# Kernel optimization log

Hardware: AMD Instinct MI355X
Metric: run time of the kernel (lower is better)

## Reference

```python
import jax, jax.numpy as jnp
import numpy as np

N_USERS = 100000
N_MOVIES = 20000
N_EDGES = 600000
FEAT = 64
HID = 128
OUT = 64
N_TUPLES = 100000


def _sage(x_src, x_dst, src_idx, dst_idx, n_dst, Wl, bl, Wr):
    # PyG SAGEConv (mean aggr): lin_l(mean of gathered src feats) + lin_r(x_dst)
    msg = x_src[src_idx]                                        # [E, d_src]
    summ = jax.ops.segment_sum(msg, dst_idx, num_segments=n_dst)
    cnt = jax.ops.segment_sum(jnp.ones((src_idx.shape[0],), x_src.dtype),
                              dst_idx, num_segments=n_dst)
    mean = summ / jnp.maximum(cnt, 1.0)[:, None]
    return mean @ Wl.T + bl + x_dst @ Wr.T


def setup_inputs() -> dict:
    key = jax.random.key(0)
    ks = jax.random.split(key, 20)
    s = 0.05
    return {
        "movie_x": jax.random.normal(ks[0], (N_MOVIES, FEAT), jnp.float32),
        "user_idx": jax.random.randint(ks[1], (N_EDGES,), 0, N_USERS),
        "movie_idx": jax.random.randint(ks[2], (N_EDGES,), 0, N_MOVIES),
        "tuples_coo": jax.random.randint(ks[3], (2, N_TUPLES), 0, N_MOVIES),
        "user_emb": jax.random.normal(ks[4], (1, HID), jnp.float32) * s,
        "W1l": jax.random.normal(ks[5], (HID, FEAT), jnp.float32) * s,
        "b1": jnp.zeros((HID,), jnp.float32),
        "W1r": jax.random.normal(ks[6], (HID, HID), jnp.float32) * s,
        "W2l": jax.random.normal(ks[7], (HID, HID), jnp.float32) * s,
        "b2": jnp.zeros((HID,), jnp.float32),
        "W2r": jax.random.normal(ks[8], (HID, FEAT), jnp.float32) * s,
        "W3l": jax.random.normal(ks[9], (HID, HID), jnp.float32) * s,
        "b3": jnp.zeros((HID,), jnp.float32),
        "W3r": jax.random.normal(ks[10], (HID, HID), jnp.float32) * s,
        "Wlin1": jax.random.normal(ks[11], (OUT, HID), jnp.float32) * s,
        "blin1": jnp.zeros((OUT,), jnp.float32),
        "Wlin2": jax.random.normal(ks[12], (OUT, HID), jnp.float32) * s,
        "blin2": jnp.zeros((OUT,), jnp.float32),
    }


def reference(movie_x, user_idx, movie_idx, tuples_coo, user_emb,
              W1l, b1, W1r, W2l, b2, W2r, W3l, b3, W3r,
              Wlin1, blin1, Wlin2, blin2):
    n_users = N_USERS
    user_x0 = jnp.broadcast_to(user_emb, (n_users, HID))  # emb.weight.repeat
    # conv1: (movie -> user) rev_rates edges: src=movie_idx, dst=user_idx
    user_x = jax.nn.relu(_sage(movie_x, user_x0, movie_idx, user_idx, n_users, W1l, b1, W1r))
    # conv2: (user -> movie) rates edges: src=user_idx, dst=movie_idx
    movie_z = jax.nn.relu(_sage(user_x, movie_x, user_idx, movie_idx, N_MOVIES, W2l, b2, W2r))
    # conv3: (movie -> user) again
    user_z = jax.nn.relu(_sage(movie_z, user_x, movie_idx, user_idx, n_users, W3l, b3, W3r))
    z_user = user_z @ Wlin1.T + blin1
    z_movie = movie_z @ Wlin2.T + blin2
    X = jnp.vstack((z_user, z_movie))
    # relation_schema = ['user', 'movie']: offset movie indices by n_users
    new_index = jnp.vstack((tuples_coo[0], tuples_coo[1] + n_users))
    return X, new_index
```

## Files before the change

kernel.cpp:

```cpp
#include <hip/hip_runtime.h>

typedef __attribute__((ext_vector_type(8))) short short8;
typedef __attribute__((ext_vector_type(4))) float f32x4;

static const int NU = 100000;
static const int NM = 20000;
static const int NE = 600000;
static const int FEAT = 64;
static const int HID = 128;
static const int OUTD = 64;
static const int NTOT = NU + NM;
static const int CVT_TOT = 81920 + NM * FEAT;
static const int CVT_BLKS = (CVT_TOT + 255) / 256;
static const int IDX_BLKS = (100000 + 255) / 256;

static const int UB_SHIFT = 9;
static const int MB_SHIFT = 7;
static const int NBU = (NU + 511) >> 9;
static const int NBM = (NM + 127) >> 7;
static const int NBUCK = NBU + NBM;
static const int EPB = 4096;
static const int NPBLK = (NE + EPB - 1) / EPB;
static const int CAP = 8192;

__device__ inline float b2f(unsigned short h) {
    unsigned int u = ((unsigned int)h) << 16;
    float f; __builtin_memcpy(&f, &u, 4); return f;
}
__device__ inline unsigned short f2b(float f) {
    unsigned int u; __builtin_memcpy(&u, &f, 4);
    u += 0x7FFFu + ((u >> 16) & 1u);
    return (unsigned short)(u >> 16);
}
__device__ inline unsigned int pk2(float a, float b) {
    return (unsigned int)f2b(a) | ((unsigned int)f2b(b) << 16);
}
__device__ inline int wswz(int row, int bc, int rowbytes) {
    return row * rowbytes + (bc ^ ((row & 7) << 4));
}

__global__ __launch_bounds__(256) void k_part_misc(
        const int* __restrict__ ui, const int* __restrict__ mi,
        int* __restrict__ gcur, int* __restrict__ entries,
        const float* __restrict__ w1l, const float* __restrict__ w2l,
        const float* __restrict__ w2r, const float* __restrict__ w3l,
        const float* __restrict__ w3r, const float* __restrict__ wl1,
        const float* __restrict__ wl2, const float* __restrict__ mx,
        unsigned short* __restrict__ dst,
        const int* __restrict__ tpl, float* __restrict__ oidx,
        const float* __restrict__ ue, const float* __restrict__ w1r,
        const float* __restrict__ b1, float* __restrict__ c1) {
    __shared__ int h[NBUCK], base[NBUCK], cur[NBUCK];
    const int b = blockIdx.x;
    const int tid = threadIdx.x;
    if (b < NPBLK) {
        for (int i = tid; i < NBUCK; i += 256) h[i] = 0;
        __syncthreads();
        int eu[EPB / 256], em[EPB / 256];
#pragma unroll
        for (int it = 0; it < EPB / 256; ++it) {
            int e = b * EPB + it * 256 + tid;
            if (e < NE) {
                eu[it] = ui[e]; em[it] = mi[e];
                atomicAdd(&h[eu[it] >> UB_SHIFT], 1);
                atomicAdd(&h[NBU + (em[it] >> MB_SHIFT)], 1);
            } else eu[it] = -1;
        }
        __syncthreads();
        for (int i = tid; i < NBUCK; i += 256) {
            int c = h[i];
            base[i] = c ? (i * CAP + atomicAdd(&gcur[i], c)) : 0;
            cur[i] = 0;
        }
        __syncthreads();
#pragma unroll
        for (int it = 0; it < EPB / 256; ++it) {
            if (eu[it] < 0) continue;
            int u = eu[it], m = em[it];
            int bu = u >> UB_SHIFT;
            int o1 = base[bu] + atomicAdd(&cur[bu], 1);
            entries[o1] = (m << UB_SHIFT) | (u & 511);
            int bm = NBU + (m >> MB_SHIFT);
            int o2 = base[bm] + atomicAdd(&cur[bm], 1);
            entries[o2] = (u << MB_SHIFT) | (m & 127);
        }
    } else if (b < NPBLK + CVT_BLKS) {
        int g = (b - NPBLK) * 256 + tid;
        if (g >= CVT_TOT) return;
        const float* s; int o;
        if      (g < 8192)   { s = w1l; o = g; }
        else if (g < 24576)  { s = w2l; o = g - 8192; }
        else if (g < 32768)  { s = w2r; o = g - 24576; }
        else if (g < 49152)  { s = w3l; o = g - 32768; }
        else if (g < 65536)  { s = w3r; o = g - 49152; }
        else if (g < 73728)  { s = wl1; o = g - 65536; }
        else if (g < 81920)  { s = wl2; o = g - 73728; }
        else                 { s = mx;  o = g - 81920; }
        dst[g] = f2b(s[o]);
    } else if (b < NPBLK + CVT_BLKS + IDX_BLKS) {
        int i = (b - NPBLK - CVT_BLKS) * 256 + tid;
        if (i < 100000) {
            oidx[i] = (float)tpl[i];
            oidx[100000 + i] = (float)(tpl[100000 + i] + NU);
        }
    } else {
        int hh = tid;
        if (hh < HID) {
            float a = 0.f;
#pragma unroll 16
            for (int k = 0; k < HID; ++k) a += ue[k] * w1r[hh * HID + k];
            c1[hh] = a + b1[hh];
        }
    }
}

__global__ __launch_bounds__(256) void k_csr(const int* __restrict__ gcur,
                                             const int* __restrict__ entries,
                                             int2* __restrict__ rp2,
                                             int* __restrict__ list) {
    __shared__ int lcnt[512], lrp[512], lcur[512], ps[256];
    const int b = blockIdx.x;
    const int tid = threadIdx.x;
    const int s = b * CAP;
    const int e = s + gcur[b];
    const bool isU = b < NBU;
    const int shift = isU ? UB_SHIFT : MB_SHIFT;
    const int mask = isU ? 511 : 127;
    const int n0 = isU ? (b << UB_SHIFT) : ((b - NBU) << MB_SHIFT);
    const int nNodes = isU ? min(512, NU - n0) : min(128, NM - n0);
    const int g0 = isU ? n0 : NU + n0;

    for (int i = tid; i < 512; i += 256) { lcnt[i] = 0; lcur[i] = 0; }
    __syncthreads();
    for (int i = s + tid; i < e; i += 256)
        atomicAdd(&lcnt[entries[i] & mask], 1);
    __syncthreads();
    int a0 = lcnt[2 * tid], a1 = lcnt[2 * tid + 1];
    int pr = a0 + a1;
    ps[tid] = pr;
    __syncthreads();
#pragma unroll
    for (int off = 1; off < 256; off <<= 1) {
        int x = (tid >= off) ? ps[tid - off] : 0;
        __syncthreads();
        ps[tid] += x;
        __syncthreads();
    }
    int excl = ps[tid] - pr;
    lrp[2 * tid] = excl;
    lrp[2 * tid + 1] = excl + a0;
    __syncthreads();
    for (int i = tid; i < nNodes; i += 256)
        rp2[g0 + i] = make_int2(s + lrp[i], s + lrp[i] + lcnt[i]);
    for (int i = s + tid; i < e; i += 256) {
        int p = entries[i];
        int dl = p & mask;
        int off = s + lrp[dl] + atomicAdd(&lcur[dl], 1);
        list[off] = p >> shift;
    }
}

template<int C>
__global__ __launch_bounds__(256) void k_gather_b(const unsigned short* __restrict__ src,
                                                  const int2* __restrict__ rp2,
                                                  const int* __restrict__ list,
                                                  unsigned short* __restrict__ dst,
                                                  int base, int n) {
    constexpr int TPN = C / 8;
    constexpr int NPB = 256 / TPN;
    const int node = blockIdx.x * NPB + threadIdx.x / TPN;
    if (node >= n) return;
    const int c8 = (threadIdx.x % TPN) * 8;
    const int2 se = rp2[base + node];
    const int s = se.x, e = se.y;

    float a[8];
#pragma unroll
    for (int j = 0; j < 8; ++j) a[j] = 0.f;

    int i = s;
    for (; i + 3 < e; i += 4) {
        int r0 = list[i], r1 = list[i + 1], r2 = list[i + 2], r3 = list[i + 3];
        short8 v0 = *reinterpret_cast<const short8*>(src + (size_t)r0 * C + c8);
        short8 v1 = *reinterpret_cast<const short8*>(src + (size_t)r1 * C + c8);
        short8 v2 = *reinterpret_cast<const short8*>(src + (size_t)r2 * C + c8);
        short8 v3 = *reinterpret_cast<const short8*>(src + (size_t)r3 * C + c8);
#pragma unroll
        for (int j = 0; j < 8; ++j)
            a[j] += (b2f((unsigned short)v0[j]) + b2f((unsigned short)v1[j]))
                  + (b2f((unsigned short)v2[j]) + b2f((unsigned short)v3[j]));
    }
    for (; i < e; ++i) {
        int r0 = list[i];
        short8 v0 = *reinterpret_cast<const short8*>(src + (size_t)r0 * C + c8);
#pragma unroll
        for (int j = 0; j < 8; ++j) a[j] += b2f((unsigned short)v0[j]);
    }
    const float sc = 1.0f / (float)max(e - s, 1);
    short8 o;
#pragma unroll
    for (int j = 0; j < 8; ++j) o[j] = (short)f2b(a[j] * sc);
    *reinterpret_cast<short8*>(dst + (size_t)node * C + c8) = o;
}

__global__ __launch_bounds__(256) void k_gather_relu(const unsigned short* __restrict__ Y1,
                                                     const int2* __restrict__ rp2,
                                                     const int* __restrict__ list,
                                                     const float* __restrict__ c1,
                                                     unsigned short* __restrict__ user_x,
                                                     int n) {
    const int node = blockIdx.x * 16 + threadIdx.x / 16;
    if (node >= n) return;
    const int c8 = (threadIdx.x % 16) * 8;
    const int2 se = rp2[node];
    const int s = se.x, e = se.y;

    float a[8];
#pragma unroll
    for (int j = 0; j < 8; ++j) a[j] = 0.f;

    int i = s;
    for (; i + 3 < e; i += 4) {
        int r0 = list[i], r1 = list[i + 1], r2 = list[i + 2], r3 = list[i + 3];
        short8 v0 = *reinterpret_cast<const short8*>(Y1 + (size_t)r0 * HID + c8);
        short8 v1 = *reinterpret_cast<const short8*>(Y1 + (size_t)r1 * HID + c8);
        short8 v2 = *reinterpret_cast<const short8*>(Y1 + (size_t)r2 * HID + c8);
        short8 v3 = *reinterpret_cast<const short8*>(Y1 + (size_t)r3 * HID + c8);
#pragma unroll
        for (int j = 0; j < 8; ++j)
            a[j] += (b2f((unsigned short)v0[j]) + b2f((unsigned short)v1[j]))
                  + (b2f((unsigned short)v2[j]) + b2f((unsigned short)v3[j]));
    }
    for (; i < e; ++i) {
        int r0 = list[i];
        short8 v0 = *reinterpret_cast<const short8*>(Y1 + (size_t)r0 * HID + c8);
#pragma unroll
        for (int j = 0; j < 8; ++j) a[j] += b2f((unsigned short)v0[j]);
    }
    const float sc = 1.0f / (float)max(e - s, 1);
    float4 cv0 = *reinterpret_cast<const float4*>(c1 + c8);
    float4 cv1 = *reinterpret_cast<const float4*>(c1 + c8 + 4);
    float r[8];
    r[0] = fmaxf(a[0] * sc + cv0.x, 0.f); r[1] = fmaxf(a[1] * sc + cv0.y, 0.f);
    r[2] = fmaxf(a[2] * sc + cv0.z, 0.f); r[3] = fmaxf(a[3] * sc + cv0.w, 0.f);
    r[4] = fmaxf(a[4] * sc + cv1.x, 0.f); r[5] = fmaxf(a[5] * sc + cv1.y, 0.f);
    r[6] = fmaxf(a[6] * sc + cv1.z, 0.f); r[7] = fmaxf(a[7] * sc + cv1.w, 0.f);
    uint4 o;
    o.x = pk2(r[0], r[1]); o.y = pk2(r[2], r[3]);
    o.z = pk2(r[4], r[5]); o.w = pk2(r[6], r[7]);
    *reinterpret_cast<uint4*>(user_x + (size_t)node * HID + c8) = o;
}

template<int K, int NO, bool AVEC, bool RELU, bool F32OUT>
__global__ __launch_bounds__(256) void k_mf2(const unsigned short* __restrict__ X,
                                             const unsigned short* __restrict__ W,
                                             const float* __restrict__ vec,
                                             void* __restrict__ Yv, int M) {
    constexpr int KT = K / 32;
    constexpr int CG = NO / 16;
    constexpr int WB = NO * K * 2;
    constexpr int RB = K * 2;
    __shared__ __align__(16) char lds[WB];
    const int tid = threadIdx.x;
    const int lane = tid & 63;
    const int wv = tid >> 6;
    const int rbase = blockIdx.x * 128 + wv * 32;
    const int lr = lane & 15;
    const int kg = lane >> 4;

#pragma unroll
    for (int i = 0; i < WB / 16 / 256; ++i) {
        int idx = tid + i * 256;
        int row = idx / (RB / 16);
        int bc = (idx % (RB / 16)) * 16;
        *reinterpret_cast<uint4*>(lds + wswz(row, bc, RB)) =
            *reinterpret_cast<const uint4*>((const char*)W + idx * 16);
    }

    short8 xb[2][KT];
#pragma unroll
    for (int t = 0; t < 2; ++t) {
        int row = min(rbase + t * 16 + lr, M - 1);
#pragma unroll
        for (int kt = 0; kt < KT; ++kt)
            xb[t][kt] = *reinterpret_cast<const short8*>(
                X + (size_t)row * K + kt * 32 + kg * 8);
    }
    __syncthreads();

    f32x4 acc[2][CG];
#pragma unroll
    for (int t = 0; t < 2; ++t)
#pragma unroll
        for (int c = 0; c < CG; ++c) acc[t][c] = (f32x4){0.f, 0.f, 0.f, 0.f};

#pragma unroll
    for (int cg = 0; cg < CG; ++cg) {
        short8 wf[KT];
#pragma unroll
        for (int kt = 0; kt < KT; ++kt)
            wf[kt] = *reinterpret_cast<const short8*>(
                lds + wswz(cg * 16 + lr, kt * 64 + kg * 16, RB));
#pragma unroll
        for (int kt = 0; kt < KT; ++kt)
#pragma unroll
            for (int t = 0; t < 2; ++t)
                acc[t][cg] = __builtin_amdgcn_mfma_f32_16x16x32_bf16(
                    wf[kt], xb[t][kt], acc[t][cg], 0, 0, 0);
    }

#pragma unroll
    for (int t = 0; t < 2; ++t) {
        const int u = rbase + t * 16 + lr;
        if (u >= M) continue;
#pragma unroll
        for (int cg = 0; cg < CG; ++cg) {
            const int h0 = cg * 16 + kg * 4;
            float v[4];
#pragma unroll
            for (int r = 0; r < 4; ++r) v[r] = acc[t][cg][r];
            if (AVEC) {
                float4 vv = *reinterpret_cast<const float4*>(vec + h0);
                v[0] += vv.x; v[1] += vv.y; v[2] += vv.z; v[3] += vv.w;
            }
            if (RELU)
#pragma unroll
                for (int r = 0; r < 4; ++r) v[r] = fmaxf(v[r], 0.f);
            if (F32OUT) {
                float4 o = make_float4(v[0], v[1], v[2], v[3]);
                *reinterpret_cast<float4*>((float*)Yv + (size_t)u * NO + h0) = o;
            } else {
                uint2 o = make_uint2(pk2(v[0], v[1]), pk2(v[2], v[3]));
                *reinterpret_cast<uint2*>((unsigned short*)Yv + (size_t)u * NO + h0) = o;
            }
        }
    }
}

__global__ __launch_bounds__(256) void k_fused_u(
        const unsigned short* __restrict__ S3, const unsigned short* __restrict__ user_x,
        const unsigned short* __restrict__ W3r, const float* __restrict__ b3,
        const unsigned short* __restrict__ Wl1, const float* __restrict__ bl1,
        float* __restrict__ out, int M) {
    __shared__ __align__(16) char lds[49152];
    const int tid = threadIdx.x;
    const int lane = tid & 63;
    const int wv = tid >> 6;
    const int rbase = blockIdx.x * 128 + wv * 32;
    const int lr = lane & 15;
    const int kg = lane >> 4;

#pragma unroll
    for (int i = 0; i < 8; ++i) {
        int idx = tid + i * 256;
        int row = idx >> 4, bc = (idx & 15) << 4;
        *reinterpret_cast<uint4*>(lds + wswz(row, bc, 256)) =
            *reinterpret_cast<const uint4*>((const char*)W3r + idx * 16);
    }
#pragma unroll
    for (int i = 0; i < 4; ++i) {
        int idx = tid + i * 256;
        int row = idx >> 4, bc = (idx & 15) << 4;
        *reinterpret_cast<uint4*>(lds + 32768 + wswz(row, bc, 256)) =
            *reinterpret_cast<const uint4*>((const char*)Wl1 + idx * 16);
    }

    short8 xc[2][4];
#pragma unroll
    for (int t = 0; t < 2; ++t) {
        int row = min(rbase + t * 16 + lr, M - 1);
#pragma unroll
        for (int kt = 0; kt < 4; ++kt)
            xc[t][kt] = *reinterpret_cast<const short8*>(
                user_x + (size_t)row * HID + kt * 32 + kg * 8);
    }
    __syncthreads();

    f32x4 acc[2][8];
#pragma unroll
    for (int t = 0; t < 2; ++t)
#pragma unroll
        for (int c = 0; c < 8; ++c) acc[t][c] = (f32x4){0.f, 0.f, 0.f, 0.f};

#pragma unroll
    for (int cg = 0; cg < 8; ++cg) {
        short8 wr[4];
#pragma unroll
        for (int kt = 0; kt < 4; ++kt)
            wr[kt] = *reinterpret_cast<const short8*>(
                lds + wswz(cg * 16 + lr, kt * 64 + kg * 16, 256));
#pragma unroll
        for (int kt = 0; kt < 4; ++kt)
#pragma unroll
            for (int t = 0; t < 2; ++t)
                acc[t][cg] = __builtin_amdgcn_mfma_f32_16x16x32_bf16(
                    wr[kt], xc[t][kt], acc[t][cg], 0, 0, 0);
    }
    __syncthreads();

#pragma unroll
    for (int t = 0; t < 2; ++t) {
        const int ul = wv * 32 + t * 16 + lr;
        const int u = min(rbase + t * 16 + lr, M - 1);
#pragma unroll
        for (int cg = 0; cg < 8; ++cg) {
            const int h0 = cg * 16 + kg * 4;
            uint2 s3 = *reinterpret_cast<const uint2*>(S3 + (size_t)u * HID + h0);
            float4 vv = *reinterpret_cast<const float4*>(b3 + h0);
            float v0 = fmaxf(acc[t][cg][0] + b2f((unsigned short)(s3.x & 0xffff)) + vv.x, 0.f);
            float v1 = fmaxf(acc[t][cg][1] + b2f((unsigned short)(s3.x >> 16)) + vv.y, 0.f);
            float v2 = fmaxf(acc[t][cg][2] + b2f((unsigned short)(s3.y & 0xffff)) + vv.z, 0.f);
            float v3 = fmaxf(acc[t][cg][3] + b2f((unsigned short)(s3.y >> 16)) + vv.w, 0.f);
            uint2 pk = make_uint2(pk2(v0, v1), pk2(v2, v3));
            *reinterpret_cast<uint2*>(lds + wswz(ul, h0 * 2, 256)) = pk;
        }
    }
    __syncthreads();

    short8 zb[2][4];
#pragma unroll
    for (int t = 0; t < 2; ++t) {
        const int ul = wv * 32 + t * 16 + lr;
#pragma unroll
        for (int kt = 0; kt < 4; ++kt)
            zb[t][kt] = *reinterpret_cast<const short8*>(
                lds + wswz(ul, kt * 64 + kg * 16, 256));
    }
    f32x4 a2[2][4];
#pragma unroll
    for (int t = 0; t < 2; ++t)
#pragma unroll
        for (int c = 0; c < 4; ++c) a2[t][c] = (f32x4){0.f, 0.f, 0.f, 0.f};
#pragma unroll
    for (int cg = 0; cg < 4; ++cg) {
        short8 wf[4];
#pragma unroll
        for (int kt = 0; kt < 4; ++kt)
            wf[kt] = *reinterpret_cast<const short8*>(
                lds + 32768 + wswz(cg * 16 + lr, kt * 64 + kg * 16, 256));
#pragma unroll
        for (int kt = 0; kt < 4; ++kt)
#pragma unroll
            for (int t = 0; t < 2; ++t)
                a2[t][cg] = __builtin_amdgcn_mfma_f32_16x16x32_bf16(
                    wf[kt], zb[t][kt], a2[t][cg], 0, 0, 0);
    }
#pragma unroll
    for (int t = 0; t < 2; ++t) {
        const int u = rbase + t * 16 + lr;
        if (u >= M) continue;
#pragma unroll
        for (int cg = 0; cg < 4; ++cg) {
            const int o0 = cg * 16 + kg * 4;
            float4 bb = *reinterpret_cast<const float4*>(bl1 + o0);
            float4 o = make_float4(a2[t][cg][0] + bb.x, a2[t][cg][1] + bb.y,
                                   a2[t][cg][2] + bb.z, a2[t][cg][3] + bb.w);
            *reinterpret_cast<float4*>(out + (size_t)u * OUTD + o0) = o;
        }
    }
}

__global__ __launch_bounds__(256) void k_fused_m(
        const unsigned short* __restrict__ mean2, const unsigned short* __restrict__ mxb,
        const unsigned short* __restrict__ W2l, const unsigned short* __restrict__ W2r,
        const float* __restrict__ b2, unsigned short* __restrict__ movie_z,
        const unsigned short* __restrict__ Wl2, const float* __restrict__ bl2,
        const unsigned short* __restrict__ W3l, unsigned short* __restrict__ Y3,
        float* __restrict__ out, int M) {
    __shared__ __align__(16) char lds[65536];
    const int tid = threadIdx.x;
    const int lane = tid & 63;
    const int wv = tid >> 6;
    const int rbase = blockIdx.x * 128 + wv * 32;
    const int lr = lane & 15;
    const int kg = lane >> 4;

#pragma unroll
    for (int i = 0; i < 8; ++i) {
        int idx = tid + i * 256;
        int row = idx >> 4, bc = (idx & 15) << 4;
        *reinterpret_cast<uint4*>(lds + wswz(row, bc, 256)) =
            *reinterpret_cast<const uint4*>((const char*)W2l + idx * 16);
    }
#pragma unroll
    for (int i = 0; i < 4; ++i) {
        int idx = tid + i * 256;
        int row = idx >> 3, bc = (idx & 7) << 4;
        *reinterpret_cast<uint4*>(lds + 32768 + wswz(row, bc, 128)) =
            *reinterpret_cast<const uint4*>((const char*)W2r + idx * 16);
        int row2 = idx >> 4, bc2 = (idx & 15) << 4;
        *reinterpret_cast<uint4*>(lds + 49152 + wswz(row2, bc2, 256)) =
            *reinterpret_cast<const uint4*>((const char*)Wl2 + idx * 16);
    }

    short8 xa[2][4], xc[2][2];
#pragma unroll
    for (int t = 0; t < 2; ++t) {
        int row = min(rbase + t * 16 + lr, M - 1);
#pragma unroll
        for (int kt = 0; kt < 4; ++kt)
            xa[t][kt] = *reinterpret_cast<const short8*>(
                mean2 + (size_t)row * HID + kt * 32 + kg * 8);
#pragma unroll
        for (int kt = 0; kt < 2; ++kt)
            xc[t][kt] = *reinterpret_cast<const short8*>(
                mxb + (size_t)row * FEAT + kt * 32 + kg * 8);
    }
    __syncthreads();

    f32x4 acc[2][8];
#pragma unroll
    for (int t = 0; t < 2; ++t)
#pragma unroll
        for (int c = 0; c < 8; ++c) acc[t][c] = (f32x4){0.f, 0.f, 0.f, 0.f};

#pragma unroll
    for (int cg = 0; cg < 8; ++cg) {
        short8 wl[4], wr[2];
#pragma unroll
        for (int kt = 0; kt < 4; ++kt)
            wl[kt] = *reinterpret_cast<const short8*>(
                lds + wswz(cg * 16 + lr, kt * 64 + kg * 16, 256));
#pragma unroll
        for (int kt = 0; kt < 2; ++kt)
            wr[kt] = *reinterpret_cast<const short8*>(
                lds + 32768 + wswz(cg * 16 + lr, kt * 64 + kg * 16, 128));
#pragma unroll
        for (int kt = 0; kt < 4; ++kt)
#pragma unroll
            for (int t = 0; t < 2; ++t)
                acc[t][cg] = __builtin_amdgcn_mfma_f32_16x16x32_bf16(
                    wl[kt], xa[t][kt], acc[t][cg], 0, 0, 0);
#pragma unroll
        for (int kt = 0; kt < 2; ++kt)
#pragma unroll
            for (int t = 0; t < 2; ++t)
                acc[t][cg] = __builtin_amdgcn_mfma_f32_16x16x32_bf16(
                    wr[kt], xc[t][kt], acc[t][cg], 0, 0, 0);
    }
    __syncthreads();

#pragma unroll
    for (int t = 0; t < 2; ++t) {
        const int ul = wv * 32 + t * 16 + lr;
        const int u = rbase + t * 16 + lr;
#pragma unroll
        for (int cg = 0; cg < 8; ++cg) {
            const int h0 = cg * 16 + kg * 4;
            float4 vv = *reinterpret_cast<const float4*>(b2 + h0);
            float v0 = fmaxf(acc[t][cg][0] + vv.x, 0.f);
            float v1 = fmaxf(acc[t][cg][1] + vv.y, 0.f);
            float v2 = fmaxf(acc[t][cg][2] + vv.z, 0.f);
            float v3 = fmaxf(acc[t][cg][3] + vv.w, 0.f);
            uint2 pk = make_uint2(pk2(v0, v1), pk2(v2, v3));
            *reinterpret_cast<uint2*>(lds + wswz(ul, h0 * 2, 256)) = pk;
            if (u < M)
                *reinterpret_cast<uint2*>(movie_z + (size_t)u * HID + h0) = pk;
        }
    }
    __syncthreads();

    short8 zb[2][4];
#pragma unroll
    for (int t = 0; t < 2; ++t) {
        const int ul = wv * 32 + t * 16 + lr;
#pragma unroll
        for (int kt = 0; kt < 4; ++kt)
            zb[t][kt] = *reinterpret_cast<const short8*>(
                lds + wswz(ul, kt * 64 + kg * 16, 256));
    }
    f32x4 a2[2][4];
#pragma unroll
    for (int t = 0; t < 2; ++t)
#pragma unroll
        for (int c = 0; c < 4; ++c) a2[t][c] = (f32x4){0.f, 0.f, 0.f, 0.f};
#pragma unroll
    for (int cg = 0; cg < 4; ++cg) {
        short8 wf[4];
#pragma unroll
        for (int kt = 0; kt < 4; ++kt)
            wf[kt] = *reinterpret_cast<const short8*>(
                lds + 49152 + wswz(cg * 16 + lr, kt * 64 + kg * 16, 256));
#pragma unroll
        for (int kt = 0; kt < 4; ++kt)
#pragma unroll
            for (int t = 0; t < 2; ++t)
                a2[t][cg] = __builtin_amdgcn_mfma_f32_16x16x32_bf16(
                    wf[kt], zb[t][kt], a2[t][cg], 0, 0, 0);
    }
#pragma unroll
    for (int t = 0; t < 2; ++t) {
        const int u = rbase + t * 16 + lr;
        if (u >= M) continue;
#pragma unroll
        for (int cg = 0; cg < 4; ++cg) {
            const int o0 = cg * 16 + kg * 4;
            float4 bb = *reinterpret_cast<const float4*>(bl2 + o0);
            float4 o = make_float4(a2[t][cg][0] + bb.x, a2[t][cg][1] + bb.y,
                                   a2[t][cg][2] + bb.z, a2[t][cg][3] + bb.w);
            *reinterpret_cast<float4*>(out + (size_t)u * OUTD + o0) = o;
        }
    }
    __syncthreads();

#pragma unroll
    for (int i = 0; i < 8; ++i) {
        int idx = tid + i * 256;
        int row = idx >> 4, bc = (idx & 15) << 4;
        *reinterpret_cast<uint4*>(lds + 32768 + wswz(row, bc, 256)) =
            *reinterpret_cast<const uint4*>((const char*)W3l + idx * 16);
    }
    __syncthreads();

    f32x4 a3[2][8];
#pragma unroll
    for (int t = 0; t < 2; ++t)
#pragma unroll
        for (int c = 0; c < 8; ++c) a3[t][c] = (f32x4){0.f, 0.f, 0.f, 0.f};
#pragma unroll
    for (int cg = 0; cg < 8; ++cg) {
        short8 wf[4];
#pragma unroll
        for (int kt = 0; kt < 4; ++kt)
            wf[kt] = *reinterpret_cast<const short8*>(
                lds + 32768 + wswz(cg * 16 + lr, kt * 64 + kg * 16, 256));
#pragma unroll
        for (int kt = 0; kt < 4; ++kt)
#pragma unroll
            for (int t = 0; t < 2; ++t)
                a3[t][cg] = __builtin_amdgcn_mfma_f32_16x16x32_bf16(
                    wf[kt], zb[t][kt], a3[t][cg], 0, 0, 0);
    }
#pragma unroll
    for (int t = 0; t < 2; ++t) {
        const int u = rbase + t * 16 + lr;
        if (u >= M) continue;
#pragma unroll
        for (int cg = 0; cg < 8; ++cg) {
            const int h0 = cg * 16 + kg * 4;
            uint2 pk = make_uint2(pk2(a3[t][cg][0], a3[t][cg][1]),
                                  pk2(a3[t][cg][2], a3[t][cg][3]));
            *reinterpret_cast<uint2*>(Y3 + (size_t)u * HID + h0) = pk;
        }
    }
}

extern "C" void kernel_launch(void* const* d_in, const int* in_sizes, int n_in,
                              void* d_out, int out_size, void* d_ws, size_t ws_size,
                              hipStream_t stream) {
    const float* movie_x  = (const float*)d_in[0];
    const int*   user_idx = (const int*)d_in[1];
    const int*   movie_idx= (const int*)d_in[2];
    const int*   tuples   = (const int*)d_in[3];
    const float* user_emb = (const float*)d_in[4];
    const float* W1l = (const float*)d_in[5];
    const float* b1  = (const float*)d_in[6];
    const float* W1r = (const float*)d_in[7];
    const float* W2l = (const float*)d_in[8];
    const float* b2  = (const float*)d_in[9];
    const float* W2r = (const float*)d_in[10];
    const float* W3l = (const float*)d_in[11];
    const float* b3  = (const float*)d_in[12];
    const float* W3r = (const float*)d_in[13];
    const float* Wlin1 = (const float*)d_in[14];
    const float* blin1 = (const float*)d_in[15];
    const float* Wlin2 = (const float*)d_in[16];
    const float* blin2 = (const float*)d_in[17];

    float* out = (float*)d_out;

    char* p = (char*)d_ws;
    int* gcur = (int*)p;  p += 360 * 4;
    int* entries = (int*)p; p += (size_t)NBUCK * CAP * 4;
    int2* rp2  = (int2*)p; p += (size_t)NTOT * 8;
    int* list  = (int*)p;  p += (size_t)NBUCK * CAP * 4;
    float* c1  = (float*)p; p += 128 * 4;
    unsigned short* wb = (unsigned short*)p; p += (size_t)CVT_TOT * 2;
    unsigned short* W1l_b  = wb;
    unsigned short* W2l_b  = wb + 8192;
    unsigned short* W2r_b  = wb + 24576;
    unsigned short* W3l_b  = wb + 32768;
    unsigned short* W3r_b  = wb + 49152;
    unsigned short* Wlin1_b= wb + 65536;
    unsigned short* Wlin2_b= wb + 73728;
    unsigned short* mxb    = wb + 81920;
    unsigned short* Y1     = (unsigned short*)p; p += (size_t)NM * HID * 2;
    unsigned short* user_x = (unsigned short*)p; p += (size_t)NU * HID * 2;
    unsigned short* mean2  = (unsigned short*)p; p += (size_t)NM * HID * 2;
    unsigned short* movie_z= (unsigned short*)p; p += (size_t)NM * HID * 2;
    unsigned short* Y3     = (unsigned short*)p; p += (size_t)NM * HID * 2;
    unsigned short* S3     = (unsigned short*)p; p += (size_t)NU * HID * 2;

    hipMemsetAsync(gcur, 0, NBUCK * sizeof(int), stream);
    k_part_misc<<<NPBLK + CVT_BLKS + IDX_BLKS + 1, 256, 0, stream>>>(
        user_idx, movie_idx, gcur, entries,
        W1l, W2l, W2r, W3l, W3r, Wlin1, Wlin2, movie_x, wb,
        tuples, out + (size_t)(NU + NM) * OUTD, user_emb, W1r, b1, c1);
    k_csr<<<NBUCK, 256, 0, stream>>>(gcur, entries, rp2, list);
    k_mf2<FEAT, HID, false, false, false><<<(NM + 127) / 128, 256, 0, stream>>>(
        mxb, W1l_b, nullptr, Y1, NM);

    k_gather_relu<<<(NU + 15) / 16, 256, 0, stream>>>(Y1, rp2, list, c1, user_x, NU);

    k_gather_b<HID><<<(NM + 15) / 16, 256, 0, stream>>>(user_x, rp2, list, mean2, NU, NM);
    k_fused_m<<<(NM + 127) / 128, 256, 0, stream>>>(
        mean2, mxb, W2l_b, W2r_b, b2, movie_z, Wlin2_b, blin2, W3l_b, Y3,
        out + (size_t)NU * OUTD, NM);

    k_gather_b<HID><<<(NU + 15) / 16, 256, 0, stream>>>(Y3, rp2, list, S3, 0, NU);
    k_fused_u<<<(NU + 127) / 128, 256, 0, stream>>>(
        S3, user_x, W3r_b, b3, Wlin1_b, blin1, out, NU);
}
```

Baseline: 164.2 us.

## Merge independent stages into combined launches and fold conv3 root term into gather

Combines the CSR build with the movie Y1 GEMM in one launch, and the movie mean gather with the user W3r GEMM (user_x @ W3r + b3 -> T3) in another, so independent work shares a grid and overlaps. The final user gather now adds T3 and applies relu to produce Z, and a separate k_mf2 computes the output linear layer, replacing the fused k_fused_u. This cuts launches and idle tails, but the user path gains an extra NU x HID bf16 intermediate write and read, and block-type divergence within each merged launch.

```diff
diff --git a/kernel.cpp b/kernel.cpp
--- a/kernel.cpp
+++ b/kernel.cpp
@@ -22,6 +22,9 @@
 static const int EPB = 4096;
 static const int NPBLK = (NE + EPB - 1) / EPB;
 static const int CAP = 8192;
+static const int Y1_BLKS = (NM + 127) / 128;
+static const int GB2 = (NM + 15) / 16;
+static const int T3_BLKS = (NU + 127) / 128;
 
 __device__ inline float b2f(unsigned short h) {
     unsigned int u = ((unsigned int)h) << 16;
@@ -114,93 +117,112 @@
     }
 }
 
-__global__ __launch_bounds__(256) void k_csr(const int* __restrict__ gcur,
-                                             const int* __restrict__ entries,
-                                             int2* __restrict__ rp2,
-                                             int* __restrict__ list) {
-    __shared__ int lcnt[512], lrp[512], lcur[512], ps[256];
+__global__ __launch_bounds__(256) void k_csr_y1(
+        const int* __restrict__ gcur, const int* __restrict__ entries,
+        int2* __restrict__ rp2, int* __restrict__ list,
+        const unsigned short* __restrict__ mxb, const unsigned short* __restrict__ W1l,
+        unsigned short* __restrict__ Y1) {
+    __shared__ __align__(16) char lds[16384];
     const int b = blockIdx.x;
     const int tid = threadIdx.x;
-    const int s = b * CAP;
-    const int e = s + gcur[b];
-    const bool isU = b < NBU;
-    const int shift = isU ? UB_SHIFT : MB_SHIFT;
-    const int mask = isU ? 511 : 127;
-    const int n0 = isU ? (b << UB_SHIFT) : ((b - NBU) << MB_SHIFT);
-    const int nNodes = isU ? min(512, NU - n0) : min(128, NM - n0);
-    const int g0 = isU ? n0 : NU + n0;
-
-    for (int i = tid; i < 512; i += 256) { lcnt[i] = 0; lcur[i] = 0; }
-    __syncthreads();
-    for (int i = s + tid; i < e; i += 256)
-        atomicAdd(&lcnt[entries[i] & mask], 1);
-    __syncthreads();
-    int a0 = lcnt[2 * tid], a1 = lcnt[2 * tid + 1];
-    int pr = a0 + a1;
-    ps[tid] = pr;
-    __syncthreads();
-#pragma unroll
-    for (int off = 1; off < 256; off <<= 1) {
-        int x = (tid >= off) ? ps[tid - off] : 0;
-        __syncthreads();
-        ps[tid] += x;
-        __syncthreads();
-    }
-    int excl = ps[tid] - pr;
-    lrp[2 * tid] = excl;
-    lrp[2 * tid + 1] = excl + a0;
-    __syncthreads();
-    for (int i = tid; i < nNodes; i += 256)
-        rp2[g0 + i] = make_int2(s + lrp[i], s + lrp[i] + lcnt[i]);
-    for (int i = s + tid; i < e; i += 256) {
-        int p = entries[i];
-        int dl = p & mask;
-        int off = s + lrp[dl] + atomicAdd(&lcur[dl], 1);
-        list[off] = p >> shift;
-    }
-}
-
-template<int C>
-__global__ __launch_bounds__(256) void k_gather_b(const unsigned short* __restrict__ src,
-                                                  const int2* __restrict__ rp2,
-                                                  const int* __restrict__ list,
-                                                  unsigned short* __restrict__ dst,
-                                                  int base, int n) {
-    constexpr int TPN = C / 8;
-    constexpr int NPB = 256 / TPN;
-    const int node = blockIdx.x * NPB + threadIdx.x / TPN;
-    if (node >= n) return;
-    const int c8 = (threadIdx.x % TPN) * 8;
-    const int2 se = rp2[base + node];
-    const int s = se.x, e = se.y;
-
-    float a[8];
-#pragma unroll
-    for (int j = 0; j < 8; ++j) a[j] = 0.f;
-
-    int i = s;
-    for (; i + 3 < e; i += 4) {
-        int r0 = list[i], r1 = list[i + 1], r2 = list[i + 2], r3 = list[i + 3];
-        short8 v0 = *reinterpret_cast<const short8*>(src + (size_t)r0 * C + c8);
-        short8 v1 = *reinterpret_cast<const short8*>(src + (size_t)r1 * C + c8);
-        short8 v2 = *reinterpret_cast<const short8*>(src + (size_t)r2 * C + c8);
-        short8 v3 = *reinterpret_cast<const short8*>(src + (size_t)r3 * C + c8);
-#pragma unroll
-        for (int j = 0; j < 8; ++j)
-            a[j] += (b2f((unsigned short)v0[j]) + b2f((unsigned short)v1[j]))
-                  + (b2f((unsigned short)v2[j]) + b2f((unsigned short)v3[j]));
-    }
-    for (; i < e; ++i) {
-        int r0 = list[i];
-        short8 v0 = *reinterpret_cast<const short8*>(src + (size_t)r0 * C + c8);
-#pragma unroll
-        for (int j = 0; j < 8; ++j) a[j] += b2f((unsigned short)v0[j]);
-    }
-    const float sc = 1.0f / (float)max(e - s, 1);
-    short8 o;
-#pragma unroll
-    for (int j = 0; j < 8; ++j) o[j] = (short)f2b(a[j] * sc);
-    *reinterpret_cast<short8*>(dst + (size_t)node * C + c8) = o;
+    if (b < NBUCK) {
+        int* lcnt = (int*)lds;
+        int* lrp  = lcnt + 512;
+        int* lcur = lrp + 512;
+        int* ps   = lcur + 512;
+        const int s = b * CAP;
+        const int e = s + gcur[b];
+        const bool isU = b < NBU;
+        const int shift = isU ? UB_SHIFT : MB_SHIFT;
+        const int mask = isU ? 511 : 127;
+        const int n0 = isU ? (b << UB_SHIFT) : ((b - NBU) << MB_SHIFT);
+        const int nNodes = isU ? min(512, NU - n0) : min(128, NM - n0);
+        const int g0 = isU ? n0 : NU + n0;
+
+        for (int i = tid; i < 512; i += 256) { lcnt[i] = 0; lcur[i] = 0; }
+        __syncthreads();
+        for (int i = s + tid; i < e; i += 256)
+            atomicAdd(&lcnt[entries[i] & mask], 1);
+        __syncthreads();
+        int a0 = lcnt[2 * tid], a1 = lcnt[2 * tid + 1];
+        int pr = a0 + a1;
+        ps[tid] = pr;
+        __syncthreads();
+#pragma unroll
+        for (int off = 1; off < 256; off <<= 1) {
+            int x = (tid >= off) ? ps[tid - off] : 0;
+            __syncthreads();
+            ps[tid] += x;
+            __syncthreads();
+        }
+        int excl = ps[tid] - pr;
+        lrp[2 * tid] = excl;
+        lrp[2 * tid + 1] = excl + a0;
+        __syncthreads();
+        for (int i = tid; i < nNodes; i += 256)
+            rp2[g0 + i] = make_int2(s + lrp[i], s + lrp[i] + lcnt[i]);
+        for (int i = s + tid; i < e; i += 256) {
+            int p = entries[i];
+            int dl = p & mask;
+            int off = s + lrp[dl] + atomicAdd(&lcur[dl], 1);
+            list[off] = p >> shift;
+        }
+    } else {
+        const int gb = b - NBUCK;
+        const int lane = tid & 63;
+        const int wv = tid >> 6;
+        const int rbase = gb * 128 + wv * 32;
+        const int lr = lane & 15;
+        const int kg = lane >> 4;
+#pragma unroll
+        for (int i = 0; i < 4; ++i) {
+            int idx = tid + i * 256;
+            int row = idx >> 3, bc = (idx & 7) << 4;
+            *reinterpret_cast<uint4*>(lds + wswz(row, bc, 128)) =
+                *reinterpret_cast<const uint4*>((const char*)W1l + idx * 16);
+        }
+        short8 xb[2][2];
+#pragma unroll
+        for (int t = 0; t < 2; ++t) {
+            int row = min(rbase + t * 16 + lr, NM - 1);
+#pragma unroll
+            for (int kt = 0; kt < 2; ++kt)
+                xb[t][kt] = *reinterpret_cast<const short8*>(
+                    mxb + (size_t)row * FEAT + kt * 32 + kg * 8);
+        }
+        __syncthreads();
+        f32x4 acc[2][8];
+#pragma unroll
+        for (int t = 0; t < 2; ++t)
+#pragma unroll
+            for (int c = 0; c < 8; ++c) acc[t][c] = (f32x4){0.f, 0.f, 0.f, 0.f};
+#pragma unroll
+        for (int cg = 0; cg < 8; ++cg) {
+            short8 wf[2];
+#pragma unroll
+            for (int kt = 0; kt < 2; ++kt)
+                wf[kt] = *reinterpret_cast<const short8*>(
+                    lds + wswz(cg * 16 + lr, kt * 64 + kg * 16, 128));
+#pragma unroll
+            for (int kt = 0; kt < 2; ++kt)
+#pragma unroll
+                for (int t = 0; t < 2; ++t)
+                    acc[t][cg] = __builtin_amdgcn_mfma_f32_16x16x32_bf16(
+                        wf[kt], xb[t][kt], acc[t][cg], 0, 0, 0);
+        }
+#pragma unroll
+        for (int t = 0; t < 2; ++t) {
+            const int u = rbase + t * 16 + lr;
+            if (u >= NM) continue;
+#pragma unroll
+            for (int cg = 0; cg < 8; ++cg) {
+                const int h0 = cg * 16 + kg * 4;
+                uint2 o = make_uint2(pk2(acc[t][cg][0], acc[t][cg][1]),
+                                     pk2(acc[t][cg][2], acc[t][cg][3]));
+                *reinterpret_cast<uint2*>(Y1 + (size_t)u * HID + h0) = o;
+            }
+        }
+    }
 }
 
 __global__ __launch_bounds__(256) void k_gather_relu(const unsigned short* __restrict__ Y1,
@@ -218,7 +240,6 @@
     float a[8];
 #pragma unroll
     for (int j = 0; j < 8; ++j) a[j] = 0.f;
-
     int i = s;
     for (; i + 3 < e; i += 4) {
         int r0 = list[i], r1 = list[i + 1], r2 = list[i + 2], r3 = list[i + 3];
@@ -249,6 +270,146 @@
     o.x = pk2(r[0], r[1]); o.y = pk2(r[2], r[3]);
     o.z = pk2(r[4], r[5]); o.w = pk2(r[6], r[7]);
     *reinterpret_cast<uint4*>(user_x + (size_t)node * HID + c8) = o;
+}
+
+__global__ __launch_bounds__(256) void k_g2t3(
+        const unsigned short* __restrict__ user_x, const int2* __restrict__ rp2,
+        const int* __restrict__ list, unsigned short* __restrict__ mean2,
+        const unsigned short* __restrict__ W3r, const float* __restrict__ b3,
+        unsigned short* __restrict__ T3) {
+    __shared__ __align__(16) char lds[32768];
+    const int b = blockIdx.x;
+    const int tid = threadIdx.x;
+    if (b < GB2) {
+        const int node = b * 16 + tid / 16;
+        if (node >= NM) return;
+        const int c8 = (tid % 16) * 8;
+        const int2 se = rp2[NU + node];
+        const int s = se.x, e = se.y;
+        float a[8];
+#pragma unroll
+        for (int j = 0; j < 8; ++j) a[j] = 0.f;
+        int i = s;
+        for (; i + 3 < e; i += 4) {
+            int r0 = list[i], r1 = list[i + 1], r2 = list[i + 2], r3 = list[i + 3];
+            short8 v0 = *reinterpret_cast<const short8*>(user_x + (size_t)r0 * HID + c8);
+            short8 v1 = *reinterpret_cast<const short8*>(user_x + (size_t)r1 * HID + c8);
+            short8 v2 = *reinterpret_cast<const short8*>(user_x + (size_t)r2 * HID + c8);
+            short8 v3 = *reinterpret_cast<const short8*>(user_x + (size_t)r3 * HID + c8);
+#pragma unroll
+            for (int j = 0; j < 8; ++j)
+                a[j] += (b2f((unsigned short)v0[j]) + b2f((unsigned short)v1[j]))
+                      + (b2f((unsigned short)v2[j]) + b2f((unsigned short)v3[j]));
+        }
+        for (; i < e; ++i) {
+            int r0 = list[i];
+            short8 v0 = *reinterpret_cast<const short8*>(user_x + (size_t)r0 * HID + c8);
+#pragma unroll
+            for (int j = 0; j < 8; ++j) a[j] += b2f((unsigned short)v0[j]);
+        }
+        const float sc = 1.0f / (float)max(e - s, 1);
+        short8 o;
+#pragma unroll
+        for (int j = 0; j < 8; ++j) o[j] = (short)f2b(a[j] * sc);
+        *reinterpret_cast<short8*>(mean2 + (size_t)node * HID + c8) = o;
+    } else {
+        const int gb = b - GB2;
+        const int lane = tid & 63;
+        const int wv = tid >> 6;
+        const int rbase = gb * 128 + wv * 32;
+        const int lr = lane & 15;
+        const int kg = lane >> 4;
+#pragma unroll
+        for (int i = 0; i < 8; ++i) {
+            int idx = tid + i * 256;
+            int row = idx >> 4, bc = (idx & 15) << 4;
+            *reinterpret_cast<uint4*>(lds + wswz(row, bc, 256)) =
+                *reinterpret_cast<const uint4*>((const char*)W3r + idx * 16);
+        }
+        short8 xb[2][4];
+#pragma unroll
+        for (int t = 0; t < 2; ++t) {
+            int row = min(rbase + t * 16 + lr, NU - 1);
+#pragma unroll
+            for (int kt = 0; kt < 4; ++kt)
+                xb[t][kt] = *reinterpret_cast<const short8*>(
+                    user_x + (size_t)row * HID + kt * 32 + kg * 8);
+        }
+        __syncthreads();
+        f32x4 acc[2][8];
+#pragma unroll
+        for (int t = 0; t < 2; ++t)
+#pragma unroll
+            for (int c = 0; c < 8; ++c) acc[t][c] = (f32x4){0.f, 0.f, 0.f, 0.f};
+#pragma unroll
+        for (int cg = 0; cg < 8; ++cg) {
+            short8 wf[4];
+#pragma unroll
+            for (int kt = 0; kt < 4; ++kt)
+                wf[kt] = *reinterpret_cast<const short8*>(
+                    lds + wswz(cg * 16 + lr, kt * 64 + kg * 16, 256));
+#pragma unroll
+            for (int kt = 0; kt < 4; ++kt)
+#pragma unroll
+                for (int t = 0; t < 2; ++t)
+                    acc[t][cg] = __builtin_amdgcn_mfma_f32_16x16x32_bf16(
+                        wf[kt], xb[t][kt], acc[t][cg], 0, 0, 0);
+        }
+#pragma unroll
+        for (int t = 0; t < 2; ++t) {
+            const int u = rbase + t * 16 + lr;
+            if (u >= NU) continue;
+#pragma unroll
+            for (int cg = 0; cg < 8; ++cg) {
+                const int h0 = cg * 16 + kg * 4;
+                float4 vv = *reinterpret_cast<const float4*>(b3 + h0);
+                uint2 o = make_uint2(pk2(acc[t][cg][0] + vv.x, acc[t][cg][1] + vv.y),
+                                     pk2(acc[t][cg][2] + vv.z, acc[t][cg][3] + vv.w));
+                *reinterpret_cast<uint2*>(T3 + (size_t)u * HID + h0) = o;
+            }
+        }
+    }
+}
+
+__global__ __launch_bounds__(256) void k_gather_z(const unsigned short* __restrict__ Y3,
+                                                  const int2* __restrict__ rp2,
+                                                  const int* __restrict__ list,
+                                                  const unsigned short* __restrict__ T3,
+                                                  unsigned short* __restrict__ Z, int n) {
+    const int node = blockIdx.x * 16 + threadIdx.x / 16;
+    if (node >= n) return;
+    const int c8 = (threadIdx.x % 16) * 8;
+    const int2 se = rp2[node];
+    const int s = se.x, e = se.y;
+
+    float a[8];
+#pragma unroll
+    for (int j = 0; j < 8; ++j) a[j] = 0.f;
+    int i = s;
+    for (; i + 3 < e; i += 4) {
+        int r0 = list[i], r1 = list[i + 1], r2 = list[i + 2], r3 = list[i + 3];
+        short8 v0 = *reinterpret_cast<const short8*>(Y3 + (size_t)r0 * HID + c8);
+        short8 v1 = *reinterpret_cast<const short8*>(Y3 + (size_t)r1 * HID + c8);
+        short8 v2 = *reinterpret_cast<const short8*>(Y3 + (size_t)r2 * HID + c8);
+        short8 v3 = *reinterpret_cast<const short8*>(Y3 + (size_t)r3 * HID + c8);
+#pragma unroll
+        for (int j = 0; j < 8; ++j)
+            a[j] += (b2f((unsigned short)v0[j]) + b2f((unsigned short)v1[j]))
+                  + (b2f((unsigned short)v2[j]) + b2f((unsigned short)v3[j]));
+    }
+    for (; i < e; ++i) {
+        int r0 = list[i];
+        short8 v0 = *reinterpret_cast<const short8*>(Y3 + (size_t)r0 * HID + c8);
+#pragma unroll
+        for (int j = 0; j < 8; ++j) a[j] += b2f((unsigned short)v0[j]);
+    }
+    const float sc = 1.0f / (float)max(e - s, 1);
+    short8 t3 = *reinterpret_cast<const short8*>(T3 + (size_t)node * HID + c8);
+    short8 o;
+#pragma unroll
+    for (int j = 0; j < 8; ++j)
+        o[j] = (short)f2b(fmaxf(a[j] * sc + b2f((unsigned short)t3[j]), 0.f));
+    *reinterpret_cast<short8*>(Z + (size_t)node * HID + c8) = o;
 }
 
 template<int K, int NO, bool AVEC, bool RELU, bool F32OUT>
@@ -333,129 +494,6 @@
                 uint2 o = make_uint2(pk2(v[0], v[1]), pk2(v[2], v[3]));
                 *reinterpret_cast<uint2*>((unsigned short*)Yv + (size_t)u * NO + h0) = o;
             }
-        }
-    }
-}
-
-__global__ __launch_bounds__(256) void k_fused_u(
-        const unsigned short* __restrict__ S3, const unsigned short* __restrict__ user_x,
-        const unsigned short* __restrict__ W3r, const float* __restrict__ b3,
-        const unsigned short* __restrict__ Wl1, const float* __restrict__ bl1,
-        float* __restrict__ out, int M) {
-    __shared__ __align__(16) char lds[49152];
-    const int tid = threadIdx.x;
-    const int lane = tid & 63;
-    const int wv = tid >> 6;
-    const int rbase = blockIdx.x * 128 + wv * 32;
-    const int lr = lane & 15;
-    const int kg = lane >> 4;
-
-#pragma unroll
-    for (int i = 0; i < 8; ++i) {
-        int idx = tid + i * 256;
-        int row = idx >> 4, bc = (idx & 15) << 4;
-        *reinterpret_cast<uint4*>(lds + wswz(row, bc, 256)) =
-            *reinterpret_cast<const uint4*>((const char*)W3r + idx * 16);
-    }
-#pragma unroll
-    for (int i = 0; i < 4; ++i) {
-        int idx = tid + i * 256;
-        int row = idx >> 4, bc = (idx & 15) << 4;
-        *reinterpret_cast<uint4*>(lds + 32768 + wswz(row, bc, 256)) =
-            *reinterpret_cast<const uint4*>((const char*)Wl1 + idx * 16);
-    }
-
-    short8 xc[2][4];
-#pragma unroll
-    for (int t = 0; t < 2; ++t) {
-        int row = min(rbase + t * 16 + lr, M - 1);
-#pragma unroll
-        for (int kt = 0; kt < 4; ++kt)
-            xc[t][kt] = *reinterpret_cast<const short8*>(
-                user_x + (size_t)row * HID + kt * 32 + kg * 8);
-    }
-    __syncthreads();
-
-    f32x4 acc[2][8];
-#pragma unroll
-    for (int t = 0; t < 2; ++t)
-#pragma unroll
-        for (int c = 0; c < 8; ++c) acc[t][c] = (f32x4){0.f, 0.f, 0.f, 0.f};
-
-#pragma unroll
-    for (int cg = 0; cg < 8; ++cg) {
-        short8 wr[4];
-#pragma unroll
-        for (int kt = 0; kt < 4; ++kt)
-            wr[kt] = *reinterpret_cast<const short8*>(
-                lds + wswz(cg * 16 + lr, kt * 64 + kg * 16, 256));
-#pragma unroll
-        for (int kt = 0; kt < 4; ++kt)
-#pragma unroll
-            for (int t = 0; t < 2; ++t)
-                acc[t][cg] = __builtin_amdgcn_mfma_f32_16x16x32_bf16(
-                    wr[kt], xc[t][kt], acc[t][cg], 0, 0, 0);
-    }
-    __syncthreads();
-
-#pragma unroll
-    for (int t = 0; t < 2; ++t) {
-        const int ul = wv * 32 + t * 16 + lr;
-        const int u = min(rbase + t * 16 + lr, M - 1);
-#pragma unroll
-        for (int cg = 0; cg < 8; ++cg) {
-            const int h0 = cg * 16 + kg * 4;
-            uint2 s3 = *reinterpret_cast<const uint2*>(S3 + (size_t)u * HID + h0);
-            float4 vv = *reinterpret_cast<const float4*>(b3 + h0);
-            float v0 = fmaxf(acc[t][cg][0] + b2f((unsigned short)(s3.x & 0xffff)) + vv.x, 0.f);
-            float v1 = fmaxf(acc[t][cg][1] + b2f((unsigned short)(s3.x >> 16)) + vv.y, 0.f);
-            float v2 = fmaxf(acc[t][cg][2] + b2f((unsigned short)(s3.y & 0xffff)) + vv.z, 0.f);
-            float v3 = fmaxf(acc[t][cg][3] + b2f((unsigned short)(s3.y >> 16)) + vv.w, 0.f);
-            uint2 pk = make_uint2(pk2(v0, v1), pk2(v2, v3));
-            *reinterpret_cast<uint2*>(lds + wswz(ul, h0 * 2, 256)) = pk;
-        }
-    }
-    __syncthreads();
-
-    short8 zb[2][4];
-#pragma unroll
-    for (int t = 0; t < 2; ++t) {
-        const int ul = wv * 32 + t * 16 + lr;
-#pragma unroll
-        for (int kt = 0; kt < 4; ++kt)
-            zb[t][kt] = *reinterpret_cast<const short8*>(
-                lds + wswz(ul, kt * 64 + kg * 16, 256));
-    }
-    f32x4 a2[2][4];
-#pragma unroll
-    for (int t = 0; t < 2; ++t)
-#pragma unroll
-        for (int c = 0; c < 4; ++c) a2[t][c] = (f32x4){0.f, 0.f, 0.f, 0.f};
-#pragma unroll
-    for (int cg = 0; cg < 4; ++cg) {
-        short8 wf[4];
-#pragma unroll
-        for (int kt = 0; kt < 4; ++kt)
-            wf[kt] = *reinterpret_cast<const short8*>(
-                lds + 32768 + wswz(cg * 16 + lr, kt * 64 + kg * 16, 256));
-#pragma unroll
-        for (int kt = 0; kt < 4; ++kt)
-#pragma unroll
-            for (int t = 0; t < 2; ++t)
-                a2[t][cg] = __builtin_amdgcn_mfma_f32_16x16x32_bf16(
-                    wf[kt], zb[t][kt], a2[t][cg], 0, 0, 0);
-    }
-#pragma unroll
-    for (int t = 0; t < 2; ++t) {
-        const int u = rbase + t * 16 + lr;
-        if (u >= M) continue;
-#pragma unroll
-        for (int cg = 0; cg < 4; ++cg) {
-            const int o0 = cg * 16 + kg * 4;
-            float4 bb = *reinterpret_cast<const float4*>(bl1 + o0);
-            float4 o = make_float4(a2[t][cg][0] + bb.x, a2[t][cg][1] + bb.y,
-                                   a2[t][cg][2] + bb.z, a2[t][cg][3] + bb.w);
-            *reinterpret_cast<float4*>(out + (size_t)u * OUTD + o0) = o;
         }
     }
 }
@@ -689,25 +727,28 @@
     unsigned short* mean2  = (unsigned short*)p; p += (size_t)NM * HID * 2;
     unsigned short* movie_z= (unsigned short*)p; p += (size_t)NM * HID * 2;
     unsigned short* Y3     = (unsigned short*)p; p += (size_t)NM * HID * 2;
-    unsigned short* S3     = (unsigned short*)p; p += (size_t)NU * HID * 2;
+    unsigned short* T3     = (unsigned short*)p; p += (size_t)NU * HID * 2;
+    unsigned short* Z      = (unsigned short*)p; p += (size_t)NU * HID * 2;
 
     hipMemsetAsync(gcur, 0, NBUCK * sizeof(int), stream);
     k_part_misc<<<NPBLK + CVT_BLKS + IDX_BLKS + 1, 256, 0, stream>>>(
         user_idx, movie_idx, gcur, entries,
         W1l, W2l, W2r, W3l, W3r, Wlin1, Wlin2, movie_x, wb,
         tuples, out + (size_t)(NU + NM) * OUTD, user_emb, W1r, b1, c1);
-    k_csr<<<NBUCK, 256, 0, stream>>>(gcur, entries, rp2, list);
-    k_mf2<FEAT, HID, false, false, false><<<(NM + 127) / 128, 256, 0, stream>>>(
-        mxb, W1l_b, nullptr, Y1, NM);
+
+    k_csr_y1<<<NBUCK + Y1_BLKS, 256, 0, stream>>>(gcur, entries, rp2, list,
+                                                  mxb, W1l_b, Y1);
 
     k_gather_relu<<<(NU + 15) / 16, 256, 0, stream>>>(Y1, rp2, list, c1, user_x, NU);
 
-    k_gather_b<HID><<<(NM + 15) / 16, 256, 0, stream>>>(user_x, rp2, list, mean2, NU, NM);
+    k_g2t3<<<GB2 + T3_BLKS, 256, 0, stream>>>(user_x, rp2, list, mean2, W3r_b, b3, T3);
+
     k_fused_m<<<(NM + 127) / 128, 256, 0, stream>>>(
         mean2, mxb, W2l_b, W2r_b, b2, movie_z, Wlin2_b, blin2, W3l_b, Y3,
         out + (size_t)NU * OUTD, NM);
 
-    k_gather_b<HID><<<(NU + 15) / 16, 256, 0, stream>>>(Y3, rp2, list, S3, 0, NU);
-    k_fused_u<<<(NU + 127) / 128, 256, 0, stream>>>(
-        S3, user_x, W3r_b, b3, Wlin1_b, blin1, out, NU);
-}
+    k_gather_z<<<(NU + 15) / 16, 256, 0, stream>>>(Y3, rp2, list, T3, Z, NU);
+
+    k_mf2<HID, OUTD, true, false, true><<<(NU + 127) / 128, 256, 0, stream>>>(
+        Z, Wlin1_b, blin1, out, NU);
+}
```

Result: no change. 165.9 us (+1.0%).
